# Performance work log

Hardware: AMD Instinct MI355X
Metric: run time of the kernel (lower is better)

Reference implementation:

```python
import jax, jax.numpy as jnp
import numpy as np

W = 4  # kernel_size

def setup_inputs() -> dict:
    key = jax.random.key(0)
    k1, k2, k3, k4 = jax.random.split(key, 4)
    B, T, D, H = 4, 4096, 2048, 256
    x = jax.random.normal(k1, (B, T, D), dtype=jnp.float32)
    # stored as [in, out] (transpose of torch Linear convention)
    w1 = jax.random.normal(k2, (D, H), dtype=jnp.float32) * 0.02
    w2 = jax.random.normal(k3, (H, D * W), dtype=jnp.float32) * 0.02
    b2 = jax.random.normal(k4, (D * W,), dtype=jnp.float32) * 0.02
    return {"x": x, "w1": w1, "w2": w2, "b2": b2}

def reference(x, w1, w2, b2):
    # x: [B, T, D]
    B, T, D = x.shape
    # kernel generator: Linear -> silu -> Linear(+bias)
    h = jax.nn.silu(jnp.einsum('btd,dh->bth', x, w1))
    flat = jnp.einsum('bth,ho->bto', h, w2) + b2          # [B, T, D*W]
    kernels = flat.reshape(B, T, D, W)                    # per-token depthwise kernels
    # causal depthwise dynamic conv: out[t] = sum_w k[t, :, w] * x[t - (W-1) + w]
    xp = jnp.pad(x, ((0, 0), (W - 1, 0), (0, 0)))         # left-pad time by W-1
    out = jnp.zeros_like(x)
    for w in range(W):  # W is a small static constant (4)
        out = out + kernels[..., w] * xp[:, w:w + T, :]
    return jax.nn.silu(out)
```

## Files before the change

### kernel.cpp

```cpp
#include <hip/hip_runtime.h>

typedef unsigned short u16;
typedef unsigned int   u32;
typedef __attribute__((ext_vector_type(8))) short short8;
typedef __attribute__((ext_vector_type(4))) float floatx4;

#define T_DIM 4096
#define D_DIM 2048
#define H_DIM 256
#define M_DIM 16384
#define NFLAT 8192

__device__ __forceinline__ u16 f2bf(float f) {
  union { float f; u32 u; } c; c.f = f;
  u32 x = c.u;
  x += 0x7FFFu + ((x >> 16) & 1u);
  return (u16)(x >> 16);
}
__device__ __forceinline__ u32 pk2(float a, float b) {
  return (u32)f2bf(a) | ((u32)f2bf(b) << 16);
}

__device__ __forceinline__ void glds16(const void* g, void* l) {
  __builtin_amdgcn_global_load_lds(
      (const __attribute__((address_space(1))) void*)g,
      (__attribute__((address_space(3))) void*)l, 16, 0, 0);
}

__global__ void __launch_bounds__(256) tr_cvt_all(const float* __restrict__ w1,
                                                  u16* __restrict__ w1t,
                                                  const float* __restrict__ w2,
                                                  u16* __restrict__ w2t) {
  __shared__ u16 tile[32][33];
  int bid = blockIdx.x;
  const float* src; u16* dst; int R, C, c0, r0;
  if (bid < 512) {
    src = w1; dst = w1t; R = D_DIM; C = H_DIM;
    c0 = (bid & 7) * 32; r0 = (bid >> 3) * 32;
  } else {
    int b = bid - 512;
    src = w2; dst = w2t; R = H_DIM; C = NFLAT;
    c0 = (b & 255) * 32; r0 = (b >> 8) * 32;
  }
  const int tx = threadIdx.x & 31;
  const int ty = threadIdx.x >> 5;
  #pragma unroll
  for (int i = ty; i < 32; i += 8)
    tile[i][tx] = f2bf(src[(size_t)(r0 + i) * C + (c0 + tx)]);
  __syncthreads();
  #pragma unroll
  for (int i = ty; i < 32; i += 8)
    dst[(size_t)(c0 + i) * R + (r0 + tx)] = tile[tx][i];
}

__global__ void __launch_bounds__(256) gemm1_silu(const float* __restrict__ X,
                                                  const u16* __restrict__ Bt,
                                                  u16* __restrict__ H) {
  __shared__ __align__(16) u16 As[2][32][64];
  __shared__ __align__(16) u16 Bs[2][256][64];
  const int tid  = threadIdx.x;
  const int lane = tid & 63, l15 = lane & 15, quad = lane >> 4;
  const int wv   = tid >> 6;
  const int m0   = blockIdx.x * 32;
  const int srow = lane >> 3, sc = lane & 7;

  floatx4 acc[2][4];
  const floatx4 zf = {0.f, 0.f, 0.f, 0.f};
  #pragma unroll
  for (int i = 0; i < 2; ++i)
    #pragma unroll
    for (int j = 0; j < 4; ++j) acc[i][j] = zf;

  float4 fA[2];

#define G1_LOADA(KT)                                                          \
  {                                                                           \
    int row = tid >> 3, g = tid & 7;                                          \
    const float* xs = &X[(size_t)(m0 + row) * D_DIM + (KT) * 64 + g * 8];     \
    fA[0] = *(const float4*)xs;                                               \
    fA[1] = *(const float4*)(xs + 4);                                         \
  }

#define G1_WRITEA(BUF)                                                        \
  {                                                                           \
    int row = tid >> 3, g = tid & 7, c = g ^ (row & 7);                       \
    uint4 pk;                                                                 \
    pk.x = pk2(fA[0].x, fA[0].y);                                             \
    pk.y = pk2(fA[0].z, fA[0].w);                                             \
    pk.z = pk2(fA[1].x, fA[1].y);                                             \
    pk.w = pk2(fA[1].z, fA[1].w);                                             \
    *(uint4*)&As[BUF][row][c * 8] = pk;                                       \
  }

#define G1_STAGEB(KT, BUF)                                                    \
  _Pragma("unroll")                                                           \
  for (int ci = 0; ci < 8; ++ci) {                 \
    int ch  = wv * 8 + ci;                                                    \
    int row = ch * 8 + srow;                             \
    glds16(&Bt[(size_t)row * D_DIM + (KT) * 64 + (sc ^ (row & 7)) * 8],       \
           (char*)Bs + (BUF) * 32768 + ch * 1024);                            \
  }

  G1_LOADA(0);
  G1_STAGEB(0, 0);
  G1_WRITEA(0);
  G1_LOADA(1);
  __syncthreads();

  #pragma unroll 2
  for (int t = 0; t < 32; ++t) {
    const int b = t & 1;
    if (t + 1 < 32) {
      G1_WRITEA(b ^ 1);
      G1_STAGEB(t + 1, b ^ 1);
    }
    if (t + 2 < 32) G1_LOADA(t + 2);
    short8 af[2][2], bfr[4][2];
    #pragma unroll
    for (int ks = 0; ks < 2; ++ks) {
      #pragma unroll
      for (int mi = 0; mi < 2; ++mi) {
        int row = mi * 16 + l15;
        af[mi][ks] = *(const short8*)&As[b][row][((ks * 4 + quad) ^ (row & 7)) * 8];
      }
      #pragma unroll
      for (int ni = 0; ni < 4; ++ni) {
        int row = wv * 64 + ni * 16 + l15;
        bfr[ni][ks] = *(const short8*)&Bs[b][row][((ks * 4 + quad) ^ (row & 7)) * 8];
      }
    }
    #pragma unroll
    for (int ks = 0; ks < 2; ++ks)
      #pragma unroll
      for (int mi = 0; mi < 2; ++mi)
        #pragma unroll
        for (int ni = 0; ni < 4; ++ni)
          acc[mi][ni] = __builtin_amdgcn_mfma_f32_16x16x32_bf16(af[mi][ks], bfr[ni][ks], acc[mi][ni], 0, 0, 0);
    if (t + 1 < 32) __syncthreads();
  }

  #pragma unroll
  for (int mi = 0; mi < 2; ++mi)
    #pragma unroll
    for (int ni = 0; ni < 4; ++ni)
      #pragma unroll
      for (int r = 0; r < 4; ++r) {
        float v = acc[mi][ni][r];
        v = v / (1.f + __expf(-v));
        int row = m0 + mi * 16 + quad * 4 + r;
        int col = wv * 64 + ni * 16 + l15;
        H[(size_t)row * H_DIM + col] = f2bf(v);
      }
#undef G1_LOADA
#undef G1_WRITEA
#undef G1_STAGEB
}

__global__ void __launch_bounds__(256) gemm2_conv_silu(const u16* __restrict__ Hin,
                                                       const u16* __restrict__ Bt,
                                                       const float* __restrict__ bias,
                                                       const float* __restrict__ X,
                                                       float* __restrict__ Out) {
  __shared__ __align__(16) u16 As[128][64];
  __shared__ __align__(16) u16 Bs[128][64];
  const int tid  = threadIdx.x;
  const int lane = tid & 63, l15 = lane & 15, quad = lane >> 4;
  const int wv   = tid >> 6, wy = wv >> 1, wx = wv & 1;
  const int m0   = blockIdx.y * 128;
  const int d0   = blockIdx.x * 32;
  const int srow = lane >> 3, sc = lane & 7;

  floatx4 acc[4][4];
  const floatx4 zf = {0.f, 0.f, 0.f, 0.f};
  #pragma unroll
  for (int i = 0; i < 4; ++i)
    #pragma unroll
    for (int j = 0; j < 4; ++j) acc[i][j] = zf;

  for (int k0 = 0; k0 < H_DIM; k0 += 64) {
    __syncthreads();
    #pragma unroll
    for (int ci = 0; ci < 4; ++ci) {
      int ch  = ci * 4 + wv;
      int row = ch * 8 + srow;
      int g   = (sc ^ (row & 7)) * 8;
      glds16(&Hin[(size_t)(m0 + row) * H_DIM + k0 + g], (char*)As + ch * 1024);
      int fc = (d0 + ((row >> 6) << 4) + (row & 15)) * 4 + ((row >> 4) & 3);
      glds16(&Bt[(size_t)fc * H_DIM + k0 + g], (char*)Bs + ch * 1024);
    }
    __syncthreads();
    short8 af[4][2], bfr[4][2];
    #pragma unroll
    for (int ks = 0; ks < 2; ++ks) {
      #pragma unroll
      for (int mi = 0; mi < 4; ++mi) {
        int row = wy * 64 + mi * 16 + l15;
        af[mi][ks] = *(const short8*)&As[row][((ks * 4 + quad) ^ (row & 7)) * 8];
      }
      #pragma unroll
      for (int ni = 0; ni < 4; ++ni) {
        int row = wx * 64 + ni * 16 + l15;
        bfr[ni][ks] = *(const short8*)&Bs[row][((ks * 4 + quad) ^ (row & 7)) * 8];
      }
    }
    #pragma unroll
    for (int ks = 0; ks < 2; ++ks)
      #pragma unroll
      for (int mi = 0; mi < 4; ++mi)
        #pragma unroll
        for (int ni = 0; ni < 4; ++ni)
          acc[mi][ni] = __builtin_amdgcn_mfma_f32_16x16x32_bf16(af[mi][ks], bfr[ni][ks], acc[mi][ni], 0, 0, 0);
  }

  const int d     = d0 + wx * 16 + l15;
  const float4 bv = *(const float4*)&bias[(size_t)d * 4];
  const int tbase = m0 & (T_DIM - 1);
  const int bbase = m0 - tbase;
  const float* xcol = &X[(size_t)bbase * D_DIM + d];
  float* ocol       = &Out[(size_t)m0 * D_DIM + d];

  #pragma unroll
  for (int mi = 0; mi < 4; ++mi) {
    int t0 = wy * 64 + mi * 16 + quad * 4;
    int tq = tbase + t0;
    float xv[7];
    #pragma unroll
    for (int j = 0; j < 7; ++j) {
      int tt = tq - 3 + j;
      xv[j] = (tt >= 0) ? xcol[(size_t)tt * D_DIM] : 0.f;
    }
    #pragma unroll
    for (int r = 0; r < 4; ++r) {
      float c0 = acc[mi][0][r] + bv.x;
      float c1 = acc[mi][1][r] + bv.y;
      float c2 = acc[mi][2][r] + bv.z;
      float c3 = acc[mi][3][r] + bv.w;
      float o  = c0 * xv[r] + c1 * xv[r + 1] + c2 * xv[r + 2] + c3 * xv[r + 3];
      float y  = o / (1.f + __expf(-o));
      ocol[(size_t)(t0 + r) * D_DIM] = y;
    }
  }
}

extern "C" void kernel_launch(void* const* d_in, const int* in_sizes, int n_in,
                              void* d_out, int out_size, void* d_ws, size_t ws_size,
                              hipStream_t stream) {
  const float* x  = (const float*)d_in[0];
  const float* w1 = (const float*)d_in[1];
  const float* w2 = (const float*)d_in[2];
  const float* b2 = (const float*)d_in[3];
  float* out = (float*)d_out;

  u16* w1t = (u16*)d_ws;
  u16* w2t = w1t + (size_t)H_DIM * D_DIM;
  u16* h   = w2t + (size_t)NFLAT * H_DIM;

  tr_cvt_all<<<512 + 2048, 256, 0, stream>>>(w1, w1t, w2, w2t);
  gemm1_silu<<<M_DIM / 32, 256, 0, stream>>>(x, w1t, h);
  gemm2_conv_silu<<<dim3(D_DIM / 32, M_DIM / 128), 256, 0, stream>>>(h, w2t, b2, x, out);
}
```

Baseline: 341.4 us.

## Deepen gemm1 A-prefetch to two tiles with explicit waitcnt and sched barriers

Restructures the gemm1 main loop so the fp32 X tiles are prefetched two iterations ahead into two alternating register sets, with the loop manually unrolled by two. __syncthreads is replaced by explicit s_waitcnt vmcnt(2)/lgkmcnt(0) plus s_barrier, and sched_barrier fences pin the order of the LDS writes, async B loads and global loads. The aim is to keep more global loads in flight across iterations instead of draining all outstanding memory operations at each barrier. In exchange it adds register pressure, and correctness now depends on the hand-counted vmcnt values matching the number of outstanding loads.

```diff
diff --git a/kernel.cpp b/kernel.cpp
--- a/kernel.cpp
+++ b/kernel.cpp
@@ -71,24 +71,24 @@
     #pragma unroll
     for (int j = 0; j < 4; ++j) acc[i][j] = zf;
 
-  float4 fA[2];
-
-#define G1_LOADA(KT)                                                          \
+  float4 fA0[2], fA1[2];
+
+#define G1_LOADA(KT, FW)                                                      \
   {                                                                           \
     int row = tid >> 3, g = tid & 7;                                          \
     const float* xs = &X[(size_t)(m0 + row) * D_DIM + (KT) * 64 + g * 8];     \
-    fA[0] = *(const float4*)xs;                                               \
-    fA[1] = *(const float4*)(xs + 4);                                         \
-  }
-
-#define G1_WRITEA(BUF)                                                        \
+    FW[0] = *(const float4*)xs;                                               \
+    FW[1] = *(const float4*)(xs + 4);                                         \
+  }
+
+#define G1_WRITEA(BUF, FW)                                                    \
   {                                                                           \
     int row = tid >> 3, g = tid & 7, c = g ^ (row & 7);                       \
     uint4 pk;                                                                 \
-    pk.x = pk2(fA[0].x, fA[0].y);                                             \
-    pk.y = pk2(fA[0].z, fA[0].w);                                             \
-    pk.z = pk2(fA[1].x, fA[1].y);                                             \
-    pk.w = pk2(fA[1].z, fA[1].w);                                             \
+    pk.x = pk2(FW[0].x, FW[0].y);                                             \
+    pk.y = pk2(FW[0].z, FW[0].w);                                             \
+    pk.z = pk2(FW[1].x, FW[1].y);                                             \
+    pk.w = pk2(FW[1].z, FW[1].w);                                             \
     *(uint4*)&As[BUF][row][c * 8] = pk;                                       \
   }
 
@@ -101,42 +101,70 @@
            (char*)Bs + (BUF) * 32768 + ch * 1024);                            \
   }
 
-  G1_LOADA(0);
+#define G1_STAGE_NEXT(T, BUFN, FW)                                            \
+  if ((T) + 1 < 32) {                                                         \
+    G1_WRITEA(BUFN, FW);                                                      \
+    __builtin_amdgcn_sched_barrier(0);                                        \
+    G1_STAGEB((T) + 1, BUFN);                                                 \
+    __builtin_amdgcn_sched_barrier(0);                                        \
+    if ((T) + 3 < 32) { G1_LOADA((T) + 3, FW); }                              \
+  }
+
+#define G1_COMPUTE(BUFC)                                                      \
+  {                                                                           \
+    short8 af[2][2], bfr[4][2];                                               \
+    _Pragma("unroll")                                                         \
+    for (int ks = 0; ks < 2; ++ks) {                                          \
+      _Pragma("unroll")                                                       \
+      for (int mi = 0; mi < 2; ++mi) {                                        \
+        int row = mi * 16 + l15;                                              \
+        af[mi][ks] = *(const short8*)&As[BUFC][row][((ks * 4 + quad) ^ (row & 7)) * 8]; \
+      }                                                                       \
+      _Pragma("unroll")                                                       \
+      for (int ni = 0; ni < 4; ++ni) {                                        \
+        int row = wv * 64 + ni * 16 + l15;                                    \
+        bfr[ni][ks] = *(const short8*)&Bs[BUFC][row][((ks * 4 + quad) ^ (row & 7)) * 8]; \
+      }                                                                       \
+    }                                                                         \
+    _Pragma("unroll")                                                         \
+    for (int ks = 0; ks < 2; ++ks)                                            \
+      _Pragma("unroll")                                                       \
+      for (int mi = 0; mi < 2; ++mi)                                          \
+        _Pragma("unroll")                                                     \
+        for (int ni = 0; ni < 4; ++ni)                                        \
+          acc[mi][ni] = __builtin_amdgcn_mfma_f32_16x16x32_bf16(af[mi][ks], bfr[ni][ks], acc[mi][ni], 0, 0, 0); \
+  }
+
+#define G1_SYNC(T)                                                            \
+  if ((T) + 1 < 32) {                                                         \
+    if ((T) <= 28) { asm volatile("s_waitcnt vmcnt(2)" ::: "memory"); }       \
+    else           { asm volatile("s_waitcnt vmcnt(0)" ::: "memory"); }       \
+    asm volatile("s_waitcnt lgkmcnt(0)" ::: "memory");                        \
+    __builtin_amdgcn_sched_barrier(0);                                        \
+    __builtin_amdgcn_s_barrier();                                             \
+    __builtin_amdgcn_sched_barrier(0);                                        \
+  }
+
+  G1_LOADA(0, fA0);
+  G1_LOADA(1, fA1);
+  G1_WRITEA(0, fA0);
+  __builtin_amdgcn_sched_barrier(0);
   G1_STAGEB(0, 0);
-  G1_WRITEA(0);
-  G1_LOADA(1);
-  __syncthreads();
-
-  #pragma unroll 2
-  for (int t = 0; t < 32; ++t) {
-    const int b = t & 1;
-    if (t + 1 < 32) {
-      G1_WRITEA(b ^ 1);
-      G1_STAGEB(t + 1, b ^ 1);
-    }
-    if (t + 2 < 32) G1_LOADA(t + 2);
-    short8 af[2][2], bfr[4][2];
-    #pragma unroll
-    for (int ks = 0; ks < 2; ++ks) {
-      #pragma unroll
-      for (int mi = 0; mi < 2; ++mi) {
-        int row = mi * 16 + l15;
-        af[mi][ks] = *(const short8*)&As[b][row][((ks * 4 + quad) ^ (row & 7)) * 8];
-      }
-      #pragma unroll
-      for (int ni = 0; ni < 4; ++ni) {
-        int row = wv * 64 + ni * 16 + l15;
-        bfr[ni][ks] = *(const short8*)&Bs[b][row][((ks * 4 + quad) ^ (row & 7)) * 8];
-      }
-    }
-    #pragma unroll
-    for (int ks = 0; ks < 2; ++ks)
-      #pragma unroll
-      for (int mi = 0; mi < 2; ++mi)
-        #pragma unroll
-        for (int ni = 0; ni < 4; ++ni)
-          acc[mi][ni] = __builtin_amdgcn_mfma_f32_16x16x32_bf16(af[mi][ks], bfr[ni][ks], acc[mi][ni], 0, 0, 0);
-    if (t + 1 < 32) __syncthreads();
+  __builtin_amdgcn_sched_barrier(0);
+  G1_LOADA(2, fA0);
+  asm volatile("s_waitcnt vmcnt(2)" ::: "memory");
+  asm volatile("s_waitcnt lgkmcnt(0)" ::: "memory");
+  __builtin_amdgcn_sched_barrier(0);
+  __builtin_amdgcn_s_barrier();
+  __builtin_amdgcn_sched_barrier(0);
+
+  for (int tt = 0; tt < 32; tt += 2) {
+    G1_STAGE_NEXT(tt, 1, fA1);
+    G1_COMPUTE(0);
+    G1_SYNC(tt);
+    G1_STAGE_NEXT(tt + 1, 0, fA0);
+    G1_COMPUTE(1);
+    G1_SYNC(tt + 1);
   }
 
   #pragma unroll
@@ -154,6 +182,9 @@
 #undef G1_LOADA
 #undef G1_WRITEA
 #undef G1_STAGEB
+#undef G1_STAGE_NEXT
+#undef G1_COMPUTE
+#undef G1_SYNC
 }
 
 __global__ void __launch_bounds__(256) gemm2_conv_silu(const u16* __restrict__ Hin,
```

Result: faster. 330.2 us (-3.3%).
